# Optimization experiments

Measured on AMD Instinct MI355X. Metric: run time of the kernel, lower is better.

Reference implementation:

```python
import jax, jax.numpy as jnp
import numpy as np

B, D_IN, H, HV, A, E, HW = 16384, 512, 512, 256, 32, 8, 512

def _lin(key, fan_in, fan_out):
    k1, k2 = jax.random.split(key)
    s = 1.0 / np.sqrt(fan_in)
    W = jax.random.uniform(k1, (fan_in, fan_out), minval=-s, maxval=s, dtype=jnp.float32)
    b = jax.random.uniform(k2, (fan_out,), minval=-s, maxval=s, dtype=jnp.float32)
    return W, b

def _stack(key, n, fan_in, fan_out):
    Ws, bs = [], []
    for k in jax.random.split(key, n):
        W, b = _lin(k, fan_in, fan_out)
        Ws.append(W); bs.append(b)
    return jnp.stack(Ws), jnp.stack(bs)

def setup_inputs() -> dict:
    key = jax.random.key(0)
    ks = jax.random.split(key, 16)
    x = jax.random.normal(ks[0], (B, D_IN), dtype=jnp.float32)
    # stacked expert policy nets: in->H, H->H, H->A (tanh)
    Wp0, bp0 = _stack(ks[1], E, D_IN, H)
    Wp1, bp1 = _stack(ks[2], E, H, H)
    Wmu, bmu = _stack(ks[3], E, H, A)
    # stacked expert value nets (hardcoded 256 hidden in source): in->256, 256->256, 256->1
    Wv0, bv0 = _stack(ks[4], E, D_IN, HV)
    Wv1, bv1 = _stack(ks[5], E, HV, HV)
    Wv, bv = _stack(ks[6], E, HV, 1)
    # gating net: in->HW, HW->HW, HW->E, softmax
    Ww0, bw0 = _lin(ks[7], D_IN, HW)
    Ww1, bw1 = _lin(ks[8], HW, HW)
    Wwo, bwo = _lin(ks[9], HW, E)
    return dict(x=x, Wp0=Wp0, bp0=bp0, Wp1=Wp1, bp1=bp1, Wmu=Wmu, bmu=bmu,
                Wv0=Wv0, bv0=bv0, Wv1=Wv1, bv1=bv1, Wv=Wv, bv=bv,
                Ww0=Ww0, bw0=bw0, Ww1=Ww1, bw1=bw1, Wwo=Wwo, bwo=bwo)

def reference(x, Wp0, bp0, Wp1, bp1, Wmu, bmu, Wv0, bv0, Wv1, bv1, Wv, bv,
              Ww0, bw0, Ww1, bw1, Wwo, bwo):
    # experts as one grouped/batched GEMM over axis e
    h = jax.nn.relu(jnp.einsum('bi,eih->ebh', x, Wp0) + bp0[:, None, :])      # [E,B,H]
    h = jax.nn.relu(jnp.einsum('ebh,ehk->ebk', h, Wp1) + bp1[:, None, :])
    actions = jnp.tanh(jnp.einsum('ebh,eha->eba', h, Wmu) + bmu[:, None, :])  # [E,B,A]
    # per-expert values
    g = jax.nn.relu(jnp.einsum('bi,eih->ebh', x, Wv0) + bv0[:, None, :])      # [E,B,HV]
    g = jax.nn.relu(jnp.einsum('ebh,ehk->ebk', g, Wv1) + bv1[:, None, :])
    values = jnp.einsum('ebh,eho->ebo', g, Wv) + bv[:, None, :]               # [E,B,1]
    # gating network + softmax
    u = jax.nn.relu(x @ Ww0 + bw0)
    u = jax.nn.relu(u @ Ww1 + bw1)
    w = jax.nn.softmax(u @ Wwo + bwo, axis=-1)                                # [B,E]
    # Categorical(w).sample() with a fixed key, then per-row gather of values
    pis = jax.random.categorical(jax.random.key(42), jnp.log(w), axis=-1)     # [B] int
    v = values[pis, jnp.arange(values.shape[1])]                              # [B,1]
    return actions, v, w
```

## Files before the change

### kernel.cpp

```cpp
#include <hip/hip_runtime.h>


typedef float   f32x4 __attribute__((ext_vector_type(4)));
typedef _Float16 f16;
typedef _Float16 f16x4 __attribute__((ext_vector_type(4)));
typedef _Float16 f16x8 __attribute__((ext_vector_type(8)));

typedef __attribute__((address_space(1))) unsigned int gas_u32;
typedef __attribute__((address_space(3))) unsigned int las_u32;

__device__ __forceinline__ void gl_lds16(const void* g, void* l) {
  __builtin_amdgcn_global_load_lds((gas_u32*)g, (las_u32*)l, 16, 0, 0);
}

__device__ __forceinline__ int xcd_swz(int b, int G) {
  int q = G >> 3, r = G & 7;
  int x = b & 7, y = b >> 3;
  return (x < r ? x * (q + 1) : r * (q + 1) + (x - r) * q) + y;
}

template<int BM, int BN, int WM, int WN, int EPI>
__global__ __launch_bounds__(256, 2) void gemm2_kernel(
    const f16* __restrict__ A, const f16* __restrict__ BT,
    const float* __restrict__ bias, void* __restrict__ Cv,
    const int K, const long long sAe, const long long sCe,
    const int mT, const int nInner, const int eShift)
{
  constexpr int FM = WM / 16, FN = WN / 16;
  constexpr int WAVES_N = BN / WN;
  __shared__ __align__(16) char sm[(BM + BN) * 128];
  char* Ash = sm;
  char* Bsh = sm + BM * 128;

  const int tid = threadIdx.x;
  const int lane = tid & 63;
  const int wid = tid >> 6;

  const int L = xcd_swz(blockIdx.x, gridDim.x);
  const int nIn = L % nInner;
  const int m   = (L / nInner) % mT;
  const int eo  = L / (nInner * mT);
  const int Nreal = 1 << eShift;
  const int nv0 = (eo * nInner + nIn) * BN;
  const int e = nv0 >> eShift;
  const int col0 = nv0 & (Nreal - 1);
  const int m0 = m * BM;

  const f16* Ab = A + (size_t)sAe * e + (size_t)m0 * K;
  const f16* Bb = BT + (size_t)nv0 * K;
  const int wr = wid / WAVES_N, wc = wid % WAVES_N;

  f32x4 acc[FM][FN] = {};

  const int ksteps = K >> 6;
  for (int kt = 0; kt < ksteps; ++kt) {
    __syncthreads();
    const f16* Ak = Ab + (kt << 6);
    const f16* Bk = Bb + (kt << 6);
    for (int u = tid; u < BM * 8; u += 256) {
      int row = u >> 3;
      int kb = ((u & 7) << 4) ^ ((row & 7) << 4);
      gl_lds16(Ak + (size_t)row * K + (kb >> 1), Ash + u * 16);
    }
    for (int u = tid; u < BN * 8; u += 256) {
      int row = u >> 3;
      int kb = ((u & 7) << 4) ^ ((row & 7) << 4);
      gl_lds16(Bk + (size_t)row * K + (kb >> 1), Bsh + u * 16);
    }
    __syncthreads();

    f16x8 af[FM][2], bf[FN][2];
    const int kl = (lane >> 4) << 4;
    #pragma unroll
    for (int fm = 0; fm < FM; ++fm) {
      int row = wr * WM + fm * 16 + (lane & 15);
      int sw = (row & 7) << 4;
      af[fm][0] = *(const f16x8*)(Ash + row * 128 + (kl ^ sw));
      af[fm][1] = *(const f16x8*)(Ash + row * 128 + ((64 + kl) ^ sw));
    }
    #pragma unroll
    for (int fn = 0; fn < FN; ++fn) {
      int row = wc * WN + fn * 16 + (lane & 15);
      int sw = (row & 7) << 4;
      bf[fn][0] = *(const f16x8*)(Bsh + row * 128 + (kl ^ sw));
      bf[fn][1] = *(const f16x8*)(Bsh + row * 128 + ((64 + kl) ^ sw));
    }
    #pragma unroll
    for (int fm = 0; fm < FM; ++fm)
      #pragma unroll
      for (int fn = 0; fn < FN; ++fn) {
        acc[fm][fn] = __builtin_amdgcn_mfma_f32_16x16x32_f16(
            bf[fn][0], af[fm][0], acc[fm][fn], 0, 0, 0);
        acc[fm][fn] = __builtin_amdgcn_mfma_f32_16x16x32_f16(
            bf[fn][1], af[fm][1], acc[fm][fn], 0, 0, 0);
      }
  }

  const int rbase = m0 + wr * WM + (lane & 15);
  const int cb = wc * WN + ((lane >> 4) << 2);
  #pragma unroll
  for (int fm = 0; fm < FM; ++fm) {
    const int row = rbase + fm * 16;
    #pragma unroll
    for (int fn = 0; fn < FN; ++fn) {
      const int bcol = cb + fn * 16;
      f32x4 v = acc[fm][fn];
      f32x4 bb = *(const f32x4*)(bias + nv0 + bcol);
      if constexpr (EPI == 0) {
        f16x4 h;
        #pragma unroll
        for (int r = 0; r < 4; ++r) h[r] = (f16)fmaxf(v[r] + bb[r], 0.0f);
        *(f16x4*)((f16*)Cv + (size_t)sCe * e + (size_t)row * Nreal + col0 + bcol) = h;
      } else {
        f32x4 o;
        #pragma unroll
        for (int r = 0; r < 4; ++r) o[r] = tanhf(v[r] + bb[r]);
        *(f32x4*)((float*)Cv + (size_t)sCe * e + (size_t)row * Nreal + col0 + bcol) = o;
      }
    }
  }
}

__device__ __forceinline__ int swz32(int row) { return ((row >> 1) & 3) << 4; }

__global__ __launch_bounds__(256, 2) void gemm_gate_kernel(
    const f16* __restrict__ Ahi, const f16* __restrict__ Alo,
    const f16* __restrict__ Bhi, const f16* __restrict__ Blo,
    const float* __restrict__ bias,
    f16* __restrict__ Chi, f16* __restrict__ Clo, float* __restrict__ C32,
    const int M, const int N, const int K, const int mode)
{
  constexpr int BM = 128, BN = 128, WM = 64, WN = 64, FM = 4, FN = 4, WAVES_N = 2;
  __shared__ __align__(16) char sm[4 * 128 * 64];
  char* AH = sm;
  char* AL = sm + 8192;
  char* BH = sm + 16384;
  char* BL = sm + 24576;

  const int tid = threadIdx.x;
  const int lane = tid & 63;
  const int wid = tid >> 6;
  const int L = xcd_swz(blockIdx.x, gridDim.x);
  const int ntn = N / BN;
  const int m0 = (L / ntn) * BM;
  const int n0 = (L % ntn) * BN;
  const int wr = wid / WAVES_N, wc = wid % WAVES_N;

  f32x4 a1[FM][FN] = {};
  f32x4 a2[FM][FN] = {};

  const int ksteps = K >> 5;
  for (int kt = 0; kt < ksteps; ++kt) {
    __syncthreads();
    const size_t ko = (size_t)(kt << 5);
    for (int u = tid; u < 512; u += 256) {
      int row = u >> 2;
      int kb = ((u & 3) << 4) ^ swz32(row);
      size_t ga = (size_t)(m0 + row) * K + ko + (kb >> 1);
      size_t gb = (size_t)(n0 + row) * K + ko + (kb >> 1);
      gl_lds16(Ahi + ga, AH + u * 16);
      gl_lds16(Alo + ga, AL + u * 16);
      gl_lds16(Bhi + gb, BH + u * 16);
      gl_lds16(Blo + gb, BL + u * 16);
    }
    __syncthreads();

    f16x8 ah[FM], al[FM], bh[FN], bl[FN];
    const int kl = (lane >> 4) << 4;
    #pragma unroll
    for (int fm = 0; fm < FM; ++fm) {
      int row = wr * WM + fm * 16 + (lane & 15);
      int o = row * 64 + (kl ^ swz32(row));
      ah[fm] = *(const f16x8*)(AH + o);
      al[fm] = *(const f16x8*)(AL + o);
    }
    #pragma unroll
    for (int fn = 0; fn < FN; ++fn) {
      int row = wc * WN + fn * 16 + (lane & 15);
      int o = row * 64 + (kl ^ swz32(row));
      bh[fn] = *(const f16x8*)(BH + o);
      bl[fn] = *(const f16x8*)(BL + o);
    }
    #pragma unroll
    for (int fm = 0; fm < FM; ++fm)
      #pragma unroll
      for (int fn = 0; fn < FN; ++fn) {
        a1[fm][fn] = __builtin_amdgcn_mfma_f32_16x16x32_f16(bh[fn], ah[fm], a1[fm][fn], 0, 0, 0);
        a2[fm][fn] = __builtin_amdgcn_mfma_f32_16x16x32_f16(bh[fn], al[fm], a2[fm][fn], 0, 0, 0);
        a2[fm][fn] = __builtin_amdgcn_mfma_f32_16x16x32_f16(bl[fn], ah[fm], a2[fm][fn], 0, 0, 0);
      }
  }

  const int rbase = m0 + wr * WM + (lane & 15);
  const int cbase = n0 + wc * WN + ((lane >> 4) << 2);
  #pragma unroll
  for (int fm = 0; fm < FM; ++fm) {
    const int row = rbase + fm * 16;
    #pragma unroll
    for (int fn = 0; fn < FN; ++fn) {
      const int col = cbase + fn * 16;
      f32x4 bb = *(const f32x4*)(bias + col);
      if (mode == 0) {
        f16x4 h, l;
        #pragma unroll
        for (int r = 0; r < 4; ++r) {
          float u = fmaxf(a1[fm][fn][r] + a2[fm][fn][r] * 9.765625e-4f + bb[r], 0.0f);
          f16 hh = (f16)u;
          h[r] = hh;
          l[r] = (f16)((u - (float)hh) * 1024.0f);
        }
        *(f16x4*)(Chi + (size_t)row * N + col) = h;
        *(f16x4*)(Clo + (size_t)row * N + col) = l;
      } else {
        f32x4 o;
        #pragma unroll
        for (int r = 0; r < 4; ++r)
          o[r] = fmaxf(a1[fm][fn][r] + a2[fm][fn][r] * 9.765625e-4f + bb[r], 0.0f);
        *(f32x4*)(C32 + (size_t)row * N + col) = o;
      }
    }
  }
}

__global__ __launch_bounds__(256) void cvt_x_kernel(
    const float* __restrict__ x, f16* __restrict__ xhi, f16* __restrict__ xlo)
{
  const size_t i = ((size_t)blockIdx.x * 256 + threadIdx.x) * 4;
  f32x4 v = *(const f32x4*)(x + i);
  f16x4 h, l;
  #pragma unroll
  for (int j = 0; j < 4; ++j) {
    f16 hh = (f16)v[j];
    h[j] = hh;
    l[j] = (f16)((v[j] - (float)hh) * 1024.0f);
  }
  *(f16x4*)(xhi + i) = h;
  *(f16x4*)(xlo + i) = l;
}

__global__ __launch_bounds__(256) void transpose_f16_kernel(
    const float* __restrict__ W, f16* __restrict__ WT, const int K, const int N)
{
  __shared__ float t[32][33];
  const int e = blockIdx.z;
  const int k0 = blockIdx.x << 5, n0 = blockIdx.y << 5;
  const int tx = threadIdx.x & 31, ty = threadIdx.x >> 5;
  const float* Wp = W + (size_t)e * K * N;
  #pragma unroll
  for (int i = 0; i < 4; ++i) {
    int k = k0 + ty + i * 8, n = n0 + tx;
    if (k < K && n < N) t[ty + i * 8][tx] = Wp[(size_t)k * N + n];
  }
  __syncthreads();
  f16* Op = WT + (size_t)e * K * N;
  #pragma unroll
  for (int i = 0; i < 4; ++i) {
    int n = n0 + ty + i * 8, k = k0 + tx;
    if (n < N && k < K) Op[(size_t)n * K + k] = (f16)t[tx][ty + i * 8];
  }
}

__global__ __launch_bounds__(256) void transpose_split_kernel(
    const float* __restrict__ W, f16* __restrict__ Thi, f16* __restrict__ Tlo,
    const int K, const int N)
{
  __shared__ float t[32][33];
  const int k0 = blockIdx.x << 5, n0 = blockIdx.y << 5;
  const int tx = threadIdx.x & 31, ty = threadIdx.x >> 5;
  #pragma unroll
  for (int i = 0; i < 4; ++i) {
    int k = k0 + ty + i * 8, n = n0 + tx;
    if (k < K && n < N) t[ty + i * 8][tx] = W[(size_t)k * N + n];
  }
  __syncthreads();
  #pragma unroll
  for (int i = 0; i < 4; ++i) {
    int n = n0 + ty + i * 8, k = k0 + tx;
    if (n < N && k < K) {
      float v = t[tx][ty + i * 8];
      f16 hh = (f16)v;
      Thi[(size_t)n * K + k] = hh;
      Tlo[(size_t)n * K + k] = (f16)((v - (float)hh) * 1024.0f);
    }
  }
}

__global__ __launch_bounds__(256) void values_kernel(
    const f16* __restrict__ G2, const float* __restrict__ Wv,
    const float* __restrict__ bv, float* __restrict__ values, const int e0)
{
  const int tid = threadIdx.x, lane = tid & 63, wid = tid >> 6;
  const int gi = blockIdx.x * 4 + wid;
  const int el = gi >> 14;
  const int b = gi & 16383;
  const int eg = e0 + el;
  const f16* g = G2 + (((size_t)el << 14) + b) * 256 + (lane << 2);
  f16x4 gv = *(const f16x4*)g;
  const float* wv = Wv + ((size_t)eg << 8) + (lane << 2);
  float a = (float)gv[0] * wv[0] + (float)gv[1] * wv[1] +
            (float)gv[2] * wv[2] + (float)gv[3] * wv[3];
  #pragma unroll
  for (int off = 32; off >= 1; off >>= 1) a += __shfl_xor(a, off);
  if (lane == 0) values[((size_t)eg << 14) + b] = a + bv[eg];
}

__device__ __forceinline__ void threefry_0_42(unsigned x0, unsigned x1,
                                              unsigned& o0, unsigned& o1)
{
  const unsigned ks0 = 0u, ks1 = 42u, ks2 = 0x1BD11BDAu ^ 42u;
  x0 += ks0; x1 += ks1;
#define TF_R(r) { x0 += x1; x1 = (x1 << r) | (x1 >> (32 - r)); x1 ^= x0; }
  TF_R(13) TF_R(15) TF_R(26) TF_R(6)  x0 += ks1; x1 += ks2 + 1u;
  TF_R(17) TF_R(29) TF_R(16) TF_R(24) x0 += ks2; x1 += ks0 + 2u;
  TF_R(13) TF_R(15) TF_R(26) TF_R(6)  x0 += ks0; x1 += ks1 + 3u;
  TF_R(17) TF_R(29) TF_R(16) TF_R(24) x0 += ks1; x1 += ks2 + 4u;
  TF_R(13) TF_R(15) TF_R(26) TF_R(6)  x0 += ks2; x1 += ks0 + 5u;
#undef TF_R
  o0 = x0; o1 = x1;
}

__global__ __launch_bounds__(256) void gating_out_kernel(
    const float* __restrict__ U2, const float* __restrict__ Wwo,
    const float* __restrict__ bwo, const float* __restrict__ values,
    float* __restrict__ w_out, float* __restrict__ v_out)
{
  __shared__ float wl[4096];
  const int tid = threadIdx.x;
  for (int i = tid; i < 1024; i += 256)
    ((f32x4*)wl)[i] = ((const f32x4*)Wwo)[i];
  __syncthreads();
  const int lane = tid & 63, wid = tid >> 6;
  const int b = blockIdx.x * 4 + wid;

  const float* u = U2 + (size_t)b * 512 + lane * 8;
  f32x4 ua = *(const f32x4*)u;
  f32x4 ub = *(const f32x4*)(u + 4);
  float acc[8] = {};
  const float* wrow = wl + lane * 64;
  #pragma unroll
  for (int i = 0; i < 8; ++i) {
    float uv = (i < 4) ? ua[i] : ub[i - 4];
    #pragma unroll
    for (int ee = 0; ee < 8; ++ee) acc[ee] += uv * wrow[i * 8 + ee];
  }
  #pragma unroll
  for (int off = 32; off >= 1; off >>= 1)
    #pragma unroll
    for (int ee = 0; ee < 8; ++ee) acc[ee] += __shfl_xor(acc[ee], off);
  #pragma unroll
  for (int ee = 0; ee < 8; ++ee) acc[ee] += bwo[ee];

  float zmax = acc[0];
  #pragma unroll
  for (int ee = 1; ee < 8; ++ee) zmax = fmaxf(zmax, acc[ee]);
  float s = 0.0f;
  #pragma unroll
  for (int ee = 0; ee < 8; ++ee) s += expf(acc[ee] - zmax);

  float t0 = (lane & 1) ? acc[1] : acc[0];
  float t1 = (lane & 1) ? acc[3] : acc[2];
  float t2 = (lane & 1) ? acc[5] : acc[4];
  float t3 = (lane & 1) ? acc[7] : acc[6];
  float s0 = (lane & 2) ? t1 : t0;
  float s1 = (lane & 2) ? t3 : t2;
  float zown = (lane & 4) ? s1 : s0;

  if (lane < 8) w_out[(size_t)b * 8 + lane] = expf(zown - zmax) / s;

  unsigned idx = ((unsigned)b << 3) | (unsigned)(lane & 7);
  unsigned o0, o1;
  threefry_0_42(0u, idx, o0, o1);
  unsigned bits = o0 ^ o1;
  float f = __uint_as_float((bits >> 9) | 0x3F800000u) - 1.0f;
  f = fmaxf(f, 1.17549435e-38f);
  float g = -logf(-logf(f));
  float y = (lane < 8) ? (zown + g) : -3.0e38f;

  float best = __shfl(y, 0);
  int pi = 0;
  #pragma unroll
  for (int ee = 1; ee < 8; ++ee) {
    float ye = __shfl(y, ee);
    if (ye > best) { best = ye; pi = ee; }
  }
  if (lane == 0) v_out[b] = values[((size_t)pi << 14) + b];
}

extern "C" void kernel_launch(void* const* d_in, const int* in_sizes, int n_in,
                              void* d_out, int out_size, void* d_ws, size_t ws_size,
                              hipStream_t stream) {
  (void)in_sizes; (void)n_in; (void)out_size;
  const float* x   = (const float*)d_in[0];
  const float* Wp0 = (const float*)d_in[1];
  const float* bp0 = (const float*)d_in[2];
  const float* Wp1 = (const float*)d_in[3];
  const float* bp1 = (const float*)d_in[4];
  const float* Wmu = (const float*)d_in[5];
  const float* bmu = (const float*)d_in[6];
  const float* Wv0 = (const float*)d_in[7];
  const float* bv0 = (const float*)d_in[8];
  const float* Wv1 = (const float*)d_in[9];
  const float* bv1 = (const float*)d_in[10];
  const float* Wv  = (const float*)d_in[11];
  const float* bv  = (const float*)d_in[12];
  const float* Ww0 = (const float*)d_in[13];
  const float* bw0 = (const float*)d_in[14];
  const float* Ww1 = (const float*)d_in[15];
  const float* bw1 = (const float*)d_in[16];
  const float* Wwo = (const float*)d_in[17];
  const float* bwo = (const float*)d_in[18];

  float* out_actions = (float*)d_out;
  float* out_v = out_actions + (size_t)8 * 16384 * 32;
  float* out_w = out_v + 16384;

  char* base = (char*)d_ws;
  size_t off = 0;
  auto alloc = [&](size_t bytes) -> char* {
    char* p = base + off;
    off = (off + bytes + 255) & ~(size_t)255;
    return p;
  };

  const size_t BD2 = (size_t)16384 * 512 * 2;
  const size_t BH2 = (size_t)16384 * 256 * 2;

  f16* x16    = (f16*)alloc(BD2);
  f16* xlo    = (f16*)alloc(BD2);
  f16* Wp0T   = (f16*)alloc((size_t)8 * 512 * 512 * 2);
  f16* Wp1T   = (f16*)alloc((size_t)8 * 512 * 512 * 2);
  f16* WmuT   = (f16*)alloc((size_t)8 * 32 * 512 * 2);
  f16* Wv0T   = (f16*)alloc((size_t)8 * 256 * 512 * 2);
  f16* Wv1T   = (f16*)alloc((size_t)8 * 256 * 256 * 2);
  f16* Ww0Thi = (f16*)alloc((size_t)512 * 512 * 2);
  f16* Ww0Tlo = (f16*)alloc((size_t)512 * 512 * 2);
  f16* Ww1Thi = (f16*)alloc((size_t)512 * 512 * 2);
  f16* Ww1Tlo = (f16*)alloc((size_t)512 * 512 * 2);
  float* valuesBuf = (float*)alloc((size_t)8 * 16384 * 4);

  size_t core = off;
  int eg = 8;
  while (eg > 1 && core + (size_t)2 * eg * BD2 > ws_size) eg >>= 1;
  const int eg_v = (2 * eg > 8) ? 8 : 2 * eg;

  f16 *BIG1, *BIG2, *U1hi, *U1lo;
  float* U2;
  if (eg >= 2) {
    BIG1 = (f16*)alloc((size_t)eg * BD2);
    BIG2 = (f16*)alloc((size_t)eg * BD2);
    U1hi = BIG1;
    U1lo = BIG1 + (size_t)16384 * 512;
    U2 = (float*)BIG2;
  } else {
    BIG1 = (f16*)alloc(BD2);
    BIG2 = (f16*)alloc(BD2);
    U1hi = (f16*)alloc(BD2);
    U1lo = (f16*)alloc(BD2);
    U2 = (float*)alloc((size_t)16384 * 512 * 4);
  }
  f16* VB1 = BIG1;
  f16* VB2 = (f16*)((char*)BIG1 + (size_t)eg_v * BH2);

  dim3 blk(256);
  const long long sBD = 16384LL * 512;
  const long long sBH = 16384LL * 256;

  cvt_x_kernel<<<8192, blk, 0, stream>>>(x, x16, xlo);
  transpose_f16_kernel<<<dim3(16, 16, 8), blk, 0, stream>>>(Wp0, Wp0T, 512, 512);
  transpose_f16_kernel<<<dim3(16, 16, 8), blk, 0, stream>>>(Wp1, Wp1T, 512, 512);
  transpose_f16_kernel<<<dim3(16, 1, 8), blk, 0, stream>>>(Wmu, WmuT, 512, 32);
  transpose_f16_kernel<<<dim3(16, 8, 8), blk, 0, stream>>>(Wv0, Wv0T, 512, 256);
  transpose_f16_kernel<<<dim3(8, 8, 8), blk, 0, stream>>>(Wv1, Wv1T, 256, 256);
  transpose_split_kernel<<<dim3(16, 16, 1), blk, 0, stream>>>(Ww0, Ww0Thi, Ww0Tlo, 512, 512);
  transpose_split_kernel<<<dim3(16, 16, 1), blk, 0, stream>>>(Ww1, Ww1Thi, Ww1Tlo, 512, 512);

  for (int e0 = 0; e0 < 8; e0 += eg) {
    gemm2_kernel<128, 128, 64, 64, 0><<<128 * 4 * eg, blk, 0, stream>>>(
        x16, Wp0T + (size_t)e0 * 512 * 512, bp0 + e0 * 512, BIG1,
        512, 0, sBD, 128, 4 * eg, 9);
    gemm2_kernel<128, 128, 64, 64, 0><<<128 * 4 * eg, blk, 0, stream>>>(
        BIG1, Wp1T + (size_t)e0 * 512 * 512, bp1 + e0 * 512, BIG2,
        512, sBD, sBD, 128, 4, 9);
    gemm2_kernel<128, 32, 32, 32, 1><<<128 * eg, blk, 0, stream>>>(
        BIG2, WmuT + (size_t)e0 * 32 * 512, bmu + e0 * 32,
        out_actions + (size_t)e0 * 16384 * 32,
        512, sBD, 16384LL * 32, 128, 1, 5);
  }

  for (int e0 = 0; e0 < 8; e0 += eg_v) {
    gemm2_kernel<128, 128, 64, 64, 0><<<128 * 2 * eg_v, blk, 0, stream>>>(
        x16, Wv0T + (size_t)e0 * 256 * 512, bv0 + e0 * 256, VB1,
        512, 0, sBH, 128, 2 * eg_v, 8);
    gemm2_kernel<128, 128, 64, 64, 0><<<128 * 2 * eg_v, blk, 0, stream>>>(
        VB1, Wv1T + (size_t)e0 * 256 * 256, bv1 + e0 * 256, VB2,
        256, sBH, sBH, 128, 2, 8);
    values_kernel<<<eg_v * 4096, blk, 0, stream>>>((const f16*)VB2, Wv, bv, valuesBuf, e0);
  }

  gemm_gate_kernel<<<512, blk, 0, stream>>>(
      x16, xlo, Ww0Thi, Ww0Tlo, bw0, U1hi, U1lo, nullptr, 16384, 512, 512, 0);
  gemm_gate_kernel<<<512, blk, 0, stream>>>(
      U1hi, U1lo, Ww1Thi, Ww1Tlo, bw1, nullptr, nullptr, U2, 16384, 512, 512, 1);
  gating_out_kernel<<<4096, blk, 0, stream>>>(U2, Wwo, bwo, valuesBuf, out_w, out_v);
}
```

Measured before the change: 466.7 us.

## Double-buffer GEMM LDS, fuse prep kernels, fold split-precision gate GEMM into K-concat

The GEMM kernel now uses double-buffered LDS, so the next K tile's global-to-LDS loads are issued while MFMAs run on the current tile. It also gains separate lda/ldc strides. The x conversion and all weight transposes are merged into a single prep launch. The gating GEMMs drop the dedicated three-MFMA hi/lo kernel and instead store hi, lo and scaled-hi blocks concatenated along K, so the generic GEMM computes the compensated product with K=1536. Double buffering doubles LDS per block and may reduce occupancy, and the gate GEMMs now read three times the K data.

Result: slower. 484.2 us (+3.7%).

```diff
diff --git a/kernel.cpp b/kernel.cpp
--- a/kernel.cpp
+++ b/kernel.cpp
@@ -23,14 +23,14 @@
 __global__ __launch_bounds__(256, 2) void gemm2_kernel(
     const f16* __restrict__ A, const f16* __restrict__ BT,
     const float* __restrict__ bias, void* __restrict__ Cv,
-    const int K, const long long sAe, const long long sCe,
+    const int K, const int lda, const int ldc,
+    const long long sAe, const long long sCe,
     const int mT, const int nInner, const int eShift)
 {
   constexpr int FM = WM / 16, FN = WN / 16;
   constexpr int WAVES_N = BN / WN;
-  __shared__ __align__(16) char sm[(BM + BN) * 128];
-  char* Ash = sm;
-  char* Bsh = sm + BM * 128;
+  constexpr int HB = (BM + BN) * 128;
+  __shared__ __align__(16) char sm[2 * HB];
 
   const int tid = threadIdx.x;
   const int lane = tid & 63;
@@ -38,37 +38,51 @@
 
   const int L = xcd_swz(blockIdx.x, gridDim.x);
   const int nIn = L % nInner;
-  const int m   = (L / nInner) % mT;
-  const int eo  = L / (nInner * mT);
-  const int Nreal = 1 << eShift;
+  const int m = (L / nInner) % mT;
+  const int eo = L / (nInner * mT);
   const int nv0 = (eo * nInner + nIn) * BN;
   const int e = nv0 >> eShift;
-  const int col0 = nv0 & (Nreal - 1);
+  const int col0 = nv0 & ((1 << eShift) - 1);
   const int m0 = m * BM;
 
-  const f16* Ab = A + (size_t)sAe * e + (size_t)m0 * K;
+  const f16* Ab = A + (size_t)sAe * e + (size_t)m0 * lda;
   const f16* Bb = BT + (size_t)nv0 * K;
   const int wr = wid / WAVES_N, wc = wid % WAVES_N;
 
-  f32x4 acc[FM][FN] = {};
-
-  const int ksteps = K >> 6;
-  for (int kt = 0; kt < ksteps; ++kt) {
-    __syncthreads();
+  auto stage = [&](char* buf, int kt) {
     const f16* Ak = Ab + (kt << 6);
     const f16* Bk = Bb + (kt << 6);
-    for (int u = tid; u < BM * 8; u += 256) {
+    char* Ash = buf;
+    char* Bsh = buf + BM * 128;
+    #pragma unroll
+    for (int u0 = 0; u0 < BM * 8; u0 += 256) {
+      int u = u0 + tid;
       int row = u >> 3;
       int kb = ((u & 7) << 4) ^ ((row & 7) << 4);
-      gl_lds16(Ak + (size_t)row * K + (kb >> 1), Ash + u * 16);
-    }
-    for (int u = tid; u < BN * 8; u += 256) {
+      gl_lds16(Ak + (size_t)row * lda + (kb >> 1), Ash + u * 16);
+    }
+    #pragma unroll
+    for (int u0 = 0; u0 < BN * 8; u0 += 256) {
+      int u = u0 + tid;
       int row = u >> 3;
       int kb = ((u & 7) << 4) ^ ((row & 7) << 4);
       gl_lds16(Bk + (size_t)row * K + (kb >> 1), Bsh + u * 16);
     }
-    __syncthreads();
-
+  };
+
+  f32x4 acc[FM][FN] = {};
+  const int ksteps = K >> 6;
+
+  stage(sm, 0);
+  __syncthreads();
+
+  for (int kt = 0; kt < ksteps; ++kt) {
+    char* cbuf = sm + (kt & 1) * HB;
+    char* nbuf = sm + ((kt & 1) ^ 1) * HB;
+    if (kt + 1 < ksteps) stage(nbuf, kt + 1);
+
+    const char* Ash = cbuf;
+    const char* Bsh = cbuf + BM * 128;
     f16x8 af[FM][2], bf[FN][2];
     const int kl = (lane >> 4) << 4;
     #pragma unroll
@@ -94,6 +108,7 @@
         acc[fm][fn] = __builtin_amdgcn_mfma_f32_16x16x32_f16(
             bf[fn][1], af[fm][1], acc[fm][fn], 0, 0, 0);
       }
+    __syncthreads();
   }
 
   const int rbase = m0 + wr * WM + (lane & 15);
@@ -104,183 +119,114 @@
     #pragma unroll
     for (int fn = 0; fn < FN; ++fn) {
       const int bcol = cb + fn * 16;
+      const int col = col0 + bcol;
       f32x4 v = acc[fm][fn];
       f32x4 bb = *(const f32x4*)(bias + nv0 + bcol);
       if constexpr (EPI == 0) {
         f16x4 h;
         #pragma unroll
         for (int r = 0; r < 4; ++r) h[r] = (f16)fmaxf(v[r] + bb[r], 0.0f);
-        *(f16x4*)((f16*)Cv + (size_t)sCe * e + (size_t)row * Nreal + col0 + bcol) = h;
-      } else {
+        *(f16x4*)((f16*)Cv + (size_t)sCe * e + (size_t)row * ldc + col) = h;
+      } else if constexpr (EPI == 1) {
         f32x4 o;
         #pragma unroll
         for (int r = 0; r < 4; ++r) o[r] = tanhf(v[r] + bb[r]);
-        *(f32x4*)((float*)Cv + (size_t)sCe * e + (size_t)row * Nreal + col0 + bcol) = o;
-      }
-    }
-  }
-}
-
-__device__ __forceinline__ int swz32(int row) { return ((row >> 1) & 3) << 4; }
-
-__global__ __launch_bounds__(256, 2) void gemm_gate_kernel(
-    const f16* __restrict__ Ahi, const f16* __restrict__ Alo,
-    const f16* __restrict__ Bhi, const f16* __restrict__ Blo,
-    const float* __restrict__ bias,
-    f16* __restrict__ Chi, f16* __restrict__ Clo, float* __restrict__ C32,
-    const int M, const int N, const int K, const int mode)
-{
-  constexpr int BM = 128, BN = 128, WM = 64, WN = 64, FM = 4, FN = 4, WAVES_N = 2;
-  __shared__ __align__(16) char sm[4 * 128 * 64];
-  char* AH = sm;
-  char* AL = sm + 8192;
-  char* BH = sm + 16384;
-  char* BL = sm + 24576;
-
-  const int tid = threadIdx.x;
-  const int lane = tid & 63;
-  const int wid = tid >> 6;
-  const int L = xcd_swz(blockIdx.x, gridDim.x);
-  const int ntn = N / BN;
-  const int m0 = (L / ntn) * BM;
-  const int n0 = (L % ntn) * BN;
-  const int wr = wid / WAVES_N, wc = wid % WAVES_N;
-
-  f32x4 a1[FM][FN] = {};
-  f32x4 a2[FM][FN] = {};
-
-  const int ksteps = K >> 5;
-  for (int kt = 0; kt < ksteps; ++kt) {
-    __syncthreads();
-    const size_t ko = (size_t)(kt << 5);
-    for (int u = tid; u < 512; u += 256) {
-      int row = u >> 2;
-      int kb = ((u & 3) << 4) ^ swz32(row);
-      size_t ga = (size_t)(m0 + row) * K + ko + (kb >> 1);
-      size_t gb = (size_t)(n0 + row) * K + ko + (kb >> 1);
-      gl_lds16(Ahi + ga, AH + u * 16);
-      gl_lds16(Alo + ga, AL + u * 16);
-      gl_lds16(Bhi + gb, BH + u * 16);
-      gl_lds16(Blo + gb, BL + u * 16);
-    }
-    __syncthreads();
-
-    f16x8 ah[FM], al[FM], bh[FN], bl[FN];
-    const int kl = (lane >> 4) << 4;
-    #pragma unroll
-    for (int fm = 0; fm < FM; ++fm) {
-      int row = wr * WM + fm * 16 + (lane & 15);
-      int o = row * 64 + (kl ^ swz32(row));
-      ah[fm] = *(const f16x8*)(AH + o);
-      al[fm] = *(const f16x8*)(AL + o);
-    }
-    #pragma unroll
-    for (int fn = 0; fn < FN; ++fn) {
-      int row = wc * WN + fn * 16 + (lane & 15);
-      int o = row * 64 + (kl ^ swz32(row));
-      bh[fn] = *(const f16x8*)(BH + o);
-      bl[fn] = *(const f16x8*)(BL + o);
-    }
-    #pragma unroll
-    for (int fm = 0; fm < FM; ++fm)
-      #pragma unroll
-      for (int fn = 0; fn < FN; ++fn) {
-        a1[fm][fn] = __builtin_amdgcn_mfma_f32_16x16x32_f16(bh[fn], ah[fm], a1[fm][fn], 0, 0, 0);
-        a2[fm][fn] = __builtin_amdgcn_mfma_f32_16x16x32_f16(bh[fn], al[fm], a2[fm][fn], 0, 0, 0);
-        a2[fm][fn] = __builtin_amdgcn_mfma_f32_16x16x32_f16(bl[fn], ah[fm], a2[fm][fn], 0, 0, 0);
-      }
-  }
-
-  const int rbase = m0 + wr * WM + (lane & 15);
-  const int cbase = n0 + wc * WN + ((lane >> 4) << 2);
-  #pragma unroll
-  for (int fm = 0; fm < FM; ++fm) {
-    const int row = rbase + fm * 16;
-    #pragma unroll
-    for (int fn = 0; fn < FN; ++fn) {
-      const int col = cbase + fn * 16;
-      f32x4 bb = *(const f32x4*)(bias + col);
-      if (mode == 0) {
-        f16x4 h, l;
+        *(f32x4*)((float*)Cv + (size_t)sCe * e + (size_t)row * ldc + col) = o;
+      } else if constexpr (EPI == 2) {
+        f32x4 o;
+        #pragma unroll
+        for (int r = 0; r < 4; ++r) o[r] = fmaxf(v[r] + bb[r], 0.0f);
+        *(f32x4*)((float*)Cv + (size_t)sCe * e + (size_t)row * ldc + col) = o;
+      } else {
+        f16x4 h, l, s;
         #pragma unroll
         for (int r = 0; r < 4; ++r) {
-          float u = fmaxf(a1[fm][fn][r] + a2[fm][fn][r] * 9.765625e-4f + bb[r], 0.0f);
+          float u = fmaxf(v[r] + bb[r], 0.0f);
           f16 hh = (f16)u;
+          float hv = (float)hh;
           h[r] = hh;
-          l[r] = (f16)((u - (float)hh) * 1024.0f);
+          l[r] = (f16)((u - hv) * 32.0f);
+          s[r] = (f16)(hv * 0.03125f);
         }
-        *(f16x4*)(Chi + (size_t)row * N + col) = h;
-        *(f16x4*)(Clo + (size_t)row * N + col) = l;
-      } else {
-        f32x4 o;
-        #pragma unroll
-        for (int r = 0; r < 4; ++r)
-          o[r] = fmaxf(a1[fm][fn][r] + a2[fm][fn][r] * 9.765625e-4f + bb[r], 0.0f);
-        *(f32x4*)(C32 + (size_t)row * N + col) = o;
+        f16* cp = (f16*)Cv + (size_t)row * ldc + col;
+        *(f16x4*)(cp) = h;
+        *(f16x4*)(cp + 512) = l;
+        *(f16x4*)(cp + 1024) = s;
       }
     }
   }
 }
 
-__global__ __launch_bounds__(256) void cvt_x_kernel(
-    const float* __restrict__ x, f16* __restrict__ xhi, f16* __restrict__ xlo)
-{
-  const size_t i = ((size_t)blockIdx.x * 256 + threadIdx.x) * 4;
-  f32x4 v = *(const f32x4*)(x + i);
-  f16x4 h, l;
-  #pragma unroll
-  for (int j = 0; j < 4; ++j) {
-    f16 hh = (f16)v[j];
-    h[j] = hh;
-    l[j] = (f16)((v[j] - (float)hh) * 1024.0f);
-  }
-  *(f16x4*)(xhi + i) = h;
-  *(f16x4*)(xlo + i) = l;
-}
-
-__global__ __launch_bounds__(256) void transpose_f16_kernel(
-    const float* __restrict__ W, f16* __restrict__ WT, const int K, const int N)
+__global__ __launch_bounds__(256) void prep_kernel(
+    const float* __restrict__ x, f16* __restrict__ xsplit,
+    const float* __restrict__ Wp0, f16* __restrict__ Wp0T,
+    const float* __restrict__ Wp1, f16* __restrict__ Wp1T,
+    const float* __restrict__ Wmu, f16* __restrict__ WmuT,
+    const float* __restrict__ Wv0, f16* __restrict__ Wv0T,
+    const float* __restrict__ Wv1, f16* __restrict__ Wv1T,
+    const float* __restrict__ Ww0, f16* __restrict__ Ww0T3,
+    const float* __restrict__ Ww1, f16* __restrict__ Ww1T3)
 {
   __shared__ float t[32][33];
-  const int e = blockIdx.z;
-  const int k0 = blockIdx.x << 5, n0 = blockIdx.y << 5;
-  const int tx = threadIdx.x & 31, ty = threadIdx.x >> 5;
+  const int tid = threadIdx.x;
+  int b = blockIdx.x;
+  if (b < 8192) {
+    const size_t i = ((size_t)b * 256 + tid) * 4;
+    const int row = (int)(i >> 9);
+    const int col = (int)(i & 511);
+    f32x4 v = *(const f32x4*)(x + i);
+    f16x4 h, l, s;
+    #pragma unroll
+    for (int j = 0; j < 4; ++j) {
+      f16 hh = (f16)v[j];
+      float hv = (float)hh;
+      h[j] = hh;
+      l[j] = (f16)((v[j] - hv) * 32.0f);
+      s[j] = (f16)(hv * 0.03125f);
+    }
+    f16* p = xsplit + (size_t)row * 1536 + col;
+    *(f16x4*)(p) = h;
+    *(f16x4*)(p + 512) = l;
+    *(f16x4*)(p + 1024) = s;
+    return;
+  }
+  b -= 8192;
+  const float* W;
+  f16* T;
+  bool triple = false;
+  int K, N;
+  if (b < 2048)               { W = Wp0; T = Wp0T; K = 512; N = 512; }
+  else if ((b -= 2048) < 2048){ W = Wp1; T = Wp1T; K = 512; N = 512; }
+  else if ((b -= 2048) < 128) { W = Wmu; T = WmuT; K = 512; N = 32; }
+  else if ((b -= 128) < 1024) { W = Wv0; T = Wv0T; K = 512; N = 256; }
+  else if ((b -= 1024) < 512) { W = Wv1; T = Wv1T; K = 256; N = 256; }
+  else if ((b -= 512) < 256)  { W = Ww0; T = Ww0T3; triple = true; K = 512; N = 512; }
+  else { b -= 256;              W = Ww1; T = Ww1T3; triple = true; K = 512; N = 512; }
+
+  const int kT = K >> 5, nT = N >> 5;
+  const int e = b / (kT * nT);
+  const int rem = b % (kT * nT);
+  const int k0 = (rem % kT) << 5;
+  const int n0 = (rem / kT) << 5;
+  const int tx = tid & 31, ty = tid >> 5;
   const float* Wp = W + (size_t)e * K * N;
   #pragma unroll
+  for (int i = 0; i < 4; ++i)
+    t[ty + i * 8][tx] = Wp[(size_t)(k0 + ty + i * 8) * N + n0 + tx];
+  __syncthreads();
+  #pragma unroll
   for (int i = 0; i < 4; ++i) {
-    int k = k0 + ty + i * 8, n = n0 + tx;
-    if (k < K && n < N) t[ty + i * 8][tx] = Wp[(size_t)k * N + n];
-  }
-  __syncthreads();
-  f16* Op = WT + (size_t)e * K * N;
-  #pragma unroll
-  for (int i = 0; i < 4; ++i) {
-    int n = n0 + ty + i * 8, k = k0 + tx;
-    if (n < N && k < K) Op[(size_t)n * K + k] = (f16)t[tx][ty + i * 8];
-  }
-}
-
-__global__ __launch_bounds__(256) void transpose_split_kernel(
-    const float* __restrict__ W, f16* __restrict__ Thi, f16* __restrict__ Tlo,
-    const int K, const int N)
-{
-  __shared__ float t[32][33];
-  const int k0 = blockIdx.x << 5, n0 = blockIdx.y << 5;
-  const int tx = threadIdx.x & 31, ty = threadIdx.x >> 5;
-  #pragma unroll
-  for (int i = 0; i < 4; ++i) {
-    int k = k0 + ty + i * 8, n = n0 + tx;
-    if (k < K && n < N) t[ty + i * 8][tx] = W[(size_t)k * N + n];
-  }
-  __syncthreads();
-  #pragma unroll
-  for (int i = 0; i < 4; ++i) {
-    int n = n0 + ty + i * 8, k = k0 + tx;
-    if (n < N && k < K) {
-      float v = t[tx][ty + i * 8];
-      f16 hh = (f16)v;
-      Thi[(size_t)n * K + k] = hh;
-      Tlo[(size_t)n * K + k] = (f16)((v - (float)hh) * 1024.0f);
+    const int n = n0 + ty + i * 8, k = k0 + tx;
+    float v = t[tx][ty + i * 8];
+    f16 hh = (f16)v;
+    if (!triple) {
+      T[(size_t)e * K * N + (size_t)n * K + k] = hh;
+    } else {
+      float hv = (float)hh;
+      f16* p = T + (size_t)n * 1536 + k;
+      p[0] = hh;
+      p[512] = (f16)(hv * 0.03125f);
+      p[1024] = (f16)((v - hv) * 32.0f);
     }
   }
 }
@@ -425,17 +371,14 @@
   const size_t BD2 = (size_t)16384 * 512 * 2;
   const size_t BH2 = (size_t)16384 * 256 * 2;
 
-  f16* x16    = (f16*)alloc(BD2);
-  f16* xlo    = (f16*)alloc(BD2);
+  f16* xsplit = (f16*)alloc((size_t)16384 * 1536 * 2);
   f16* Wp0T   = (f16*)alloc((size_t)8 * 512 * 512 * 2);
   f16* Wp1T   = (f16*)alloc((size_t)8 * 512 * 512 * 2);
   f16* WmuT   = (f16*)alloc((size_t)8 * 32 * 512 * 2);
   f16* Wv0T   = (f16*)alloc((size_t)8 * 256 * 512 * 2);
   f16* Wv1T   = (f16*)alloc((size_t)8 * 256 * 256 * 2);
-  f16* Ww0Thi = (f16*)alloc((size_t)512 * 512 * 2);
-  f16* Ww0Tlo = (f16*)alloc((size_t)512 * 512 * 2);
-  f16* Ww1Thi = (f16*)alloc((size_t)512 * 512 * 2);
-  f16* Ww1Tlo = (f16*)alloc((size_t)512 * 512 * 2);
+  f16* Ww0T3  = (f16*)alloc((size_t)512 * 1536 * 2);
+  f16* Ww1T3  = (f16*)alloc((size_t)512 * 1536 * 2);
   float* valuesBuf = (float*)alloc((size_t)8 * 16384 * 4);
 
   size_t core = off;
@@ -443,19 +386,17 @@
   while (eg > 1 && core + (size_t)2 * eg * BD2 > ws_size) eg >>= 1;
   const int eg_v = (2 * eg > 8) ? 8 : 2 * eg;
 
-  f16 *BIG1, *BIG2, *U1hi, *U1lo;
+  f16 *BIG1, *BIG2, *U1split;
   float* U2;
-  if (eg >= 2) {
+  if (eg >= 4) {
     BIG1 = (f16*)alloc((size_t)eg * BD2);
     BIG2 = (f16*)alloc((size_t)eg * BD2);
-    U1hi = BIG1;
-    U1lo = BIG1 + (size_t)16384 * 512;
+    U1split = BIG1;
     U2 = (float*)BIG2;
   } else {
-    BIG1 = (f16*)alloc(BD2);
-    BIG2 = (f16*)alloc(BD2);
-    U1hi = (f16*)alloc(BD2);
-    U1lo = (f16*)alloc(BD2);
+    BIG1 = (f16*)alloc((size_t)eg * BD2);
+    BIG2 = (f16*)alloc((size_t)eg * BD2);
+    U1split = (f16*)alloc((size_t)16384 * 1536 * 2);
     U2 = (float*)alloc((size_t)16384 * 512 * 4);
   }
   f16* VB1 = BIG1;
@@ -465,41 +406,38 @@
   const long long sBD = 16384LL * 512;
   const long long sBH = 16384LL * 256;
 
-  cvt_x_kernel<<<8192, blk, 0, stream>>>(x, x16, xlo);
-  transpose_f16_kernel<<<dim3(16, 16, 8), blk, 0, stream>>>(Wp0, Wp0T, 512, 512);
-  transpose_f16_kernel<<<dim3(16, 16, 8), blk, 0, stream>>>(Wp1, Wp1T, 512, 512);
-  transpose_f16_kernel<<<dim3(16, 1, 8), blk, 0, stream>>>(Wmu, WmuT, 512, 32);
-  transpose_f16_kernel<<<dim3(16, 8, 8), blk, 0, stream>>>(Wv0, Wv0T, 512, 256);
-  transpose_f16_kernel<<<dim3(8, 8, 8), blk, 0, stream>>>(Wv1, Wv1T, 256, 256);
-  transpose_split_kernel<<<dim3(16, 16, 1), blk, 0, stream>>>(Ww0, Ww0Thi, Ww0Tlo, 512, 512);
-  transpose_split_kernel<<<dim3(16, 16, 1), blk, 0, stream>>>(Ww1, Ww1Thi, Ww1Tlo, 512, 512);
+  prep_kernel<<<14464, blk, 0, stream>>>(
+      x, xsplit, Wp0, Wp0T, Wp1, Wp1T, Wmu, WmuT, Wv0, Wv0T, Wv1, Wv1T,
+      Ww0, Ww0T3, Ww1, Ww1T3);
 
   for (int e0 = 0; e0 < 8; e0 += eg) {
     gemm2_kernel<128, 128, 64, 64, 0><<<128 * 4 * eg, blk, 0, stream>>>(
-        x16, Wp0T + (size_t)e0 * 512 * 512, bp0 + e0 * 512, BIG1,
-        512, 0, sBD, 128, 4 * eg, 9);
+        xsplit, Wp0T + (size_t)e0 * 512 * 512, bp0 + e0 * 512, BIG1,
+        512, 1536, 512, 0, sBD, 128, 4 * eg, 9);
     gemm2_kernel<128, 128, 64, 64, 0><<<128 * 4 * eg, blk, 0, stream>>>(
         BIG1, Wp1T + (size_t)e0 * 512 * 512, bp1 + e0 * 512, BIG2,
-        512, sBD, sBD, 128, 4, 9);
+        512, 512, 512, sBD, sBD, 128, 4, 9);
     gemm2_kernel<128, 32, 32, 32, 1><<<128 * eg, blk, 0, stream>>>(
         BIG2, WmuT + (size_t)e0 * 32 * 512, bmu + e0 * 32,
         out_actions + (size_t)e0 * 16384 * 32,
-        512, sBD, 16384LL * 32, 128, 1, 5);
+        512, 512, 32, sBD, 16384LL * 32, 128, 1, 5);
   }
 
   for (int e0 = 0; e0 < 8; e0 += eg_v) {
     gemm2_kernel<128, 128, 64, 64, 0><<<128 * 2 * eg_v, blk, 0, stream>>>(
-        x16, Wv0T + (size_t)e0 * 256 * 512, bv0 + e0 * 256, VB1,
-        512, 0, sBH, 128, 2 * eg_v, 8);
+        xsplit, Wv0T + (size_t)e0 * 256 * 512, bv0 + e0 * 256, VB1,
+        512, 1536, 256, 0, sBH, 128, 2 * eg_v, 8);
     gemm2_kernel<128, 128, 64, 64, 0><<<128 * 2 * eg_v, blk, 0, stream>>>(
         VB1, Wv1T + (size_t)e0 * 256 * 256, bv1 + e0 * 256, VB2,
-        256, sBH, sBH, 128, 2, 8);
+        256, 256, 256, sBH, sBH, 128, 2, 8);
     values_kernel<<<eg_v * 4096, blk, 0, stream>>>((const f16*)VB2, Wv, bv, valuesBuf, e0);
   }
 
-  gemm_gate_kernel<<<512, blk, 0, stream>>>(
-      x16, xlo, Ww0Thi, Ww0Tlo, bw0, U1hi, U1lo, nullptr, 16384, 512, 512, 0);
-  gemm_gate_kernel<<<512, blk, 0, stream>>>(
-      U1hi, U1lo, Ww1Thi, Ww1Tlo, bw1, nullptr, nullptr, U2, 16384, 512, 512, 1);
+  gemm2_kernel<128, 128, 64, 64, 3><<<512, blk, 0, stream>>>(
+      xsplit, Ww0T3, bw0, U1split,
+      1536, 1536, 1536, 0, 0, 128, 4, 9);
+  gemm2_kernel<128, 128, 64, 64, 2><<<512, blk, 0, stream>>>(
+      U1split, Ww1T3, bw1, U2,
+      1536, 1536, 512, 0, 0, 128, 4, 9);
   gating_out_kernel<<<4096, blk, 0, stream>>>(U2, Wwo, bwo, valuesBuf, out_w, out_v);
 }
```
